# Kernel tuning notes

Hardware: AMD Instinct MI355X
Metric: run time of the kernel (lower is better)

## Reference

```python
import jax, jax.numpy as jnp
import numpy as np

N, D = 8192, 1024


def setup_inputs() -> dict:
    key = jax.random.key(0)
    k1, k2 = jax.random.split(key)
    x = jax.random.normal(k1, (N, D), dtype=jnp.float32)
    # scale weight like a trained linear layer (~1/sqrt(D)) so softmax isn't fully saturated
    W = jax.random.normal(k2, (D, D), dtype=jnp.float32) * (1.0 / np.sqrt(D))
    b = jnp.zeros((D,), dtype=jnp.float32)
    recency_weight = jnp.full((1,), -0.5, dtype=jnp.float32)  # nn.Parameter init in source
    return {"x": x, "W": W, "b": b, "recency_weight": recency_weight}


def reference(x, W, b, recency_weight):
    # linear + relu
    x_proj = jax.nn.relu(x @ W.T + b)          # [N, D]
    # tied self-matmul
    scores = x_proj @ x_proj.T                  # [N, N]
    n = x.shape[0]
    idx = jnp.arange(n)
    # causal mask: upper triangle strictly above diagonal (use_current_timestep=True)
    upper = idx[None, :] > idx[:, None]         # [N, N] bool
    scores = jnp.where(upper, -jnp.inf, scores)
    # recency bias: toeplitz |i - j|, zeroed on masked (upper) part, scaled by recency_weight
    dist = jnp.abs(idx[:, None] - idx[None, :]).astype(scores.dtype)
    recency = recency_weight[0] * jnp.where(upper, 0.0, dist)
    scores = scores + recency
    return jax.nn.softmax(scores, axis=1)       # [N, N] lower-triangular attention
```

## Files before the change

### kernel.cpp

```cpp
#include <hip/hip_runtime.h>
#include <math.h>

#define NR 8192
#define DIM 1024

typedef __attribute__((ext_vector_type(8))) short bf16x8;
typedef __attribute__((ext_vector_type(4))) float f32x4;

static __device__ __forceinline__ unsigned short f2bf(float f) {
  unsigned int u = __float_as_uint(f);
  u += 0x7fffu + ((u >> 16) & 1u);
  return (unsigned short)(u >> 16);
}

static __device__ __forceinline__ float bf2f(unsigned short u) {
  return __uint_as_float(((unsigned int)u) << 16);
}

static __device__ __forceinline__ void gload_lds16(const void* g, void* lds) {
  __builtin_amdgcn_global_load_lds(
      (const __attribute__((address_space(1))) unsigned int*)g,
      (__attribute__((address_space(3))) unsigned int*)lds, 16, 0, 0);
}

__global__ __launch_bounds__(256) void zerok(float* __restrict__ p, int n) {
  int i = blockIdx.x * 256 + threadIdx.x;
  if (i < n) p[i] = 0.0f;
}

__global__ __launch_bounds__(256) void cvt_bf16(const float* __restrict__ in,
                                                unsigned short* __restrict__ outp,
                                                int n4) {
  int i = blockIdx.x * 256 + threadIdx.x;
  if (i < n4) {
    float4 v = ((const float4*)in)[i];
    ushort4 o;
    o.x = f2bf(v.x); o.y = f2bf(v.y); o.z = f2bf(v.z); o.w = f2bf(v.w);
    ((ushort4*)outp)[i] = o;
  }
}

static __device__ __forceinline__ void gemm_core(const unsigned short* A,
                                                 const unsigned short* B,
                                                 int m0, int n0, int K,
                                                 short* As, short* Bs,
                                                 f32x4 acc[4][4]) {
  const int tid  = threadIdx.x;
  const int lane = tid & 63;
  const int wave = tid >> 6;
  const int wr = wave >> 1, wc = wave & 1;
  const int ch_r = lane >> 2;
  const int ch_c = (lane & 3) * 8;

  for (int kt = 0; kt < K; kt += 32) {
#pragma unroll
    for (int c = 0; c < 4; ++c) {
      int ch = wave * 4 + c;
      if (ch < 8) {
        const unsigned short* g = A + (size_t)(m0 + ch * 16 + ch_r) * DIM + kt + ch_c;
        gload_lds16(g, As + ch * 512);
      } else {
        const unsigned short* g = B + (size_t)(n0 + (ch - 8) * 16 + ch_r) * DIM + kt + ch_c;
        gload_lds16(g, Bs + (ch - 8) * 512);
      }
    }
    asm volatile("s_waitcnt vmcnt(0)" ::: "memory");
    __syncthreads();

    bf16x8 af[4], bfr[4];
#pragma unroll
    for (int m = 0; m < 4; ++m)
      af[m] = *(const bf16x8*)(As + (wr * 64 + m * 16 + (lane & 15)) * 32 + (lane >> 4) * 8);
#pragma unroll
    for (int n = 0; n < 4; ++n)
      bfr[n] = *(const bf16x8*)(Bs + (wc * 64 + n * 16 + (lane & 15)) * 32 + (lane >> 4) * 8);
#pragma unroll
    for (int m = 0; m < 4; ++m)
#pragma unroll
      for (int n = 0; n < 4; ++n)
        acc[m][n] = __builtin_amdgcn_mfma_f32_16x16x32_bf16(af[m], bfr[n], acc[m][n], 0, 0, 0);
    __syncthreads();
  }
}

__global__ __launch_bounds__(256) void gemm1_relu(const unsigned short* __restrict__ Xb,
                                                  const unsigned short* __restrict__ Wb,
                                                  const float* __restrict__ bias,
                                                  unsigned short* __restrict__ XP,
                                                  float* __restrict__ diag) {
  __shared__ short As[4096], Bs[4096];
  const int m0 = blockIdx.y * 128, n0 = blockIdx.x * 128;
  f32x4 acc[4][4] = {};
  gemm_core(Xb, Wb, m0, n0, DIM, As, Bs, acc);

  const int lane = threadIdx.x & 63, wave = threadIdx.x >> 6;
  const int wr = wave >> 1, wc = wave & 1, g = lane >> 4, li = lane & 15;
  float bv[4];
#pragma unroll
  for (int n = 0; n < 4; ++n) bv[n] = bias[n0 + wc * 64 + n * 16 + li];
#pragma unroll
  for (int m = 0; m < 4; ++m) {
#pragma unroll
    for (int r = 0; r < 4; ++r) {
      int row = m0 + wr * 64 + m * 16 + g * 4 + r;
      float ds = 0.0f;
#pragma unroll
      for (int n = 0; n < 4; ++n) {
        int col = n0 + wc * 64 + n * 16 + li;
        float v = fmaxf(acc[m][n][r] + bv[n], 0.0f);
        XP[(size_t)row * DIM + col] = f2bf(v);
        ds += v * v;
      }
#pragma unroll
      for (int off = 1; off < 16; off <<= 1) ds += __shfl_xor(ds, off);
      if (li == 0) atomicAdd(&diag[row], ds);
    }
  }
}

__global__ __launch_bounds__(256) void gemm2_scores(const unsigned short* __restrict__ XP,
                                                    const float* __restrict__ rwp,
                                                    unsigned short* __restrict__ Pb,
                                                    const float* __restrict__ diag,
                                                    float* __restrict__ Lrow) {
  int t = ((int)blockIdx.x & 7) * 260 + ((int)blockIdx.x >> 3);
  int by = (int)((sqrtf(8.0f * (float)t + 1.0f) - 1.0f) * 0.5f);
  while ((by + 1) * (by + 2) / 2 <= t) ++by;
  while (by * (by + 1) / 2 > t) --by;
  const int bx = t - by * (by + 1) / 2;

  __shared__ short As[4096], Bs[4096];
  const int m0 = by * 128, n0 = bx * 128;
  f32x4 acc[4][4] = {};
  gemm_core(XP, XP, m0, n0, DIM, As, Bs, acc);

  const float rw = rwp[0];
  const int lane = threadIdx.x & 63, wave = threadIdx.x >> 6;
  const int wr = wave >> 1, wc = wave & 1, g = lane >> 4, li = lane & 15;

#pragma unroll
  for (int m = 0; m < 4; ++m) {
#pragma unroll
    for (int r = 0; r < 4; ++r) {
      const int row = m0 + wr * 64 + m * 16 + g * 4 + r;
      const float dg = diag[row];
      float se = 0.0f;
#pragma unroll
      for (int n = 0; n < 4; ++n) {
        int col = n0 + wc * 64 + n * 16 + li;
        float v = acc[m][n][r];
        v = (col <= row) ? v + rw * (float)(row - col) : -INFINITY;
        float e = __expf(v - dg);
        se += e;
        if (col <= row) Pb[(size_t)row * NR + col] = f2bf(e);
      }
#pragma unroll
      for (int off = 1; off < 16; off <<= 1) se += __shfl_xor(se, off);
      if (li == 0) atomicAdd(&Lrow[row], se);
    }
  }
}

__global__ __launch_bounds__(256) void normk(const unsigned short* __restrict__ Pb,
                                             float* __restrict__ out,
                                             const float* __restrict__ Lrow) {
  const size_t idx = (size_t)blockIdx.x * 256 + threadIdx.x;
  const int row = (int)(idx >> 11);
  const int j0 = (int)(idx & 2047) * 4;
  float4* p = (float4*)out + idx;
  if (j0 > row) {
    float4 z; z.x = 0.f; z.y = 0.f; z.z = 0.f; z.w = 0.f;
    *p = z;
    return;
  }
  const float sc = __builtin_amdgcn_rcpf(Lrow[row]);
  ushort4 q = *(const ushort4*)(Pb + (size_t)row * NR + j0);
  float4 o;
  o.x = bf2f(q.x) * sc;
  o.y = bf2f(q.y) * sc;
  o.z = bf2f(q.z) * sc;
  o.w = bf2f(q.w) * sc;
  if (j0 + 3 > row) {
    if (j0 + 1 > row) o.y = 0.f;
    if (j0 + 2 > row) o.z = 0.f;
    o.w = 0.f;
  }
  *p = o;
}

extern "C" void kernel_launch(void* const* d_in, const int* in_sizes, int n_in,
                              void* d_out, int out_size, void* d_ws, size_t ws_size,
                              hipStream_t stream) {
  const float* x  = (const float*)d_in[0];
  const float* W  = (const float*)d_in[1];
  const float* b  = (const float*)d_in[2];
  const float* rw = (const float*)d_in[3];
  float* out = (float*)d_out;

  char* ws = (char*)d_ws;
  unsigned short* Xb = (unsigned short*)(ws);
  unsigned short* Wb = (unsigned short*)(ws + (size_t)(16 << 20));
  unsigned short* XP = (unsigned short*)(ws + (size_t)(18 << 20));
  float* diag = (float*)(ws + (size_t)(34 << 20));
  float* Lrow = (float*)(ws + (size_t)(34 << 20) + 32768);
  unsigned short* Pb = (unsigned short*)(ws + (size_t)(64 << 20));

  zerok<<<(2 * NR + 255) / 256, 256, 0, stream>>>(diag, 2 * NR);
  cvt_bf16<<<NR * DIM / 4 / 256, 256, 0, stream>>>(x, Xb, NR * DIM / 4);
  cvt_bf16<<<DIM * DIM / 4 / 256, 256, 0, stream>>>(W, Wb, DIM * DIM / 4);
  gemm1_relu<<<dim3(DIM / 128, NR / 128), 256, 0, stream>>>(Xb, Wb, b, XP, diag);
  gemm2_scores<<<2080, 256, 0, stream>>>(XP, rw, Pb, diag, Lrow);
  normk<<<(NR / 4) * (NR / 256), 256, 0, stream>>>(Pb, out, Lrow);
}
```

Measured before the change: 460.7 us.

## Add 4-stage async LDS pipeline with XOR swizzle to GEMM core

Replaces the single-buffered GEMM main loop with a 4-buffer ring that keeps three K-tiles of direct global-to-LDS loads in flight. Waits use partial vmcnt values and one barrier per iteration instead of a full drain plus two syncs. LDS chunks are XOR-swizzled on both the store and read sides to reduce bank conflicts. LDS use rises to 64KB per block, which may lower occupancy.

```diff
diff --git a/kernel.cpp b/kernel.cpp
--- a/kernel.cpp
+++ b/kernel.cpp
@@ -3,6 +3,7 @@
 
 #define NR 8192
 #define DIM 1024
+#define BK 32
 
 typedef __attribute__((ext_vector_type(8))) short bf16x8;
 typedef __attribute__((ext_vector_type(4))) float f32x4;
@@ -40,47 +41,62 @@
   }
 }
 
-static __device__ __forceinline__ void gemm_core(const unsigned short* A,
-                                                 const unsigned short* B,
-                                                 int m0, int n0, int K,
-                                                 short* As, short* Bs,
-                                                 f32x4 acc[4][4]) {
+static __device__ __forceinline__ void gemm_core_pipe(const unsigned short* A,
+                                                      const unsigned short* B,
+                                                      int m0, int n0,
+                                                      short* S,
+                                                      f32x4 acc[4][4]) {
   const int tid  = threadIdx.x;
   const int lane = tid & 63;
   const int wave = tid >> 6;
   const int wr = wave >> 1, wc = wave & 1;
-  const int ch_r = lane >> 2;
-  const int ch_c = (lane & 3) * 8;
-
-  for (int kt = 0; kt < K; kt += 32) {
-#pragma unroll
-    for (int c = 0; c < 4; ++c) {
-      int ch = wave * 4 + c;
-      if (ch < 8) {
-        const unsigned short* g = A + (size_t)(m0 + ch * 16 + ch_r) * DIM + kt + ch_c;
-        gload_lds16(g, As + ch * 512);
-      } else {
-        const unsigned short* g = B + (size_t)(n0 + (ch - 8) * 16 + ch_r) * DIM + kt + ch_c;
-        gload_lds16(g, Bs + (ch - 8) * 512);
-      }
-    }
-    asm volatile("s_waitcnt vmcnt(0)" ::: "memory");
-    __syncthreads();
-
+  const int li = lane & 15, g = lane >> 4;
+  const int r_loc = tid >> 2;
+  const int q     = (tid & 3) ^ ((r_loc >> 1) & 3);
+  const int kch = (g ^ ((li >> 1) & 3)) * 8;
+
+#define ISSUE_TILE(t_)                                                              \
+  do {                                                                              \
+    const int kt_ = (t_) * BK;                                                      \
+    short* buf_ = S + ((t_) & 3) * 8192;                                            \
+    gload_lds16(A + (size_t)(m0 +      r_loc) * DIM + kt_ + q * 8,                  \
+                buf_ + wave * 512);                                                 \
+    gload_lds16(A + (size_t)(m0 + 64 + r_loc) * DIM + kt_ + q * 8,                  \
+                buf_ + 2048 + wave * 512);                                          \
+    gload_lds16(B + (size_t)(n0 +      r_loc) * DIM + kt_ + q * 8,                  \
+                buf_ + 4096 + wave * 512);                                          \
+    gload_lds16(B + (size_t)(n0 + 64 + r_loc) * DIM + kt_ + q * 8,                  \
+                buf_ + 6144 + wave * 512);                                          \
+  } while (0)
+
+  ISSUE_TILE(0);
+  ISSUE_TILE(1);
+  ISSUE_TILE(2);
+
+  for (int t = 0; t < DIM / BK; ++t) {
+    if (t <= DIM / BK - 3)      asm volatile("s_waitcnt vmcnt(8)" ::: "memory");
+    else if (t == DIM / BK - 2) asm volatile("s_waitcnt vmcnt(4)" ::: "memory");
+    else                        asm volatile("s_waitcnt vmcnt(0)" ::: "memory");
+    __builtin_amdgcn_s_barrier();
+
+    const short* Ab = S + (t & 3) * 8192;
+    const short* Bb = Ab + 4096;
     bf16x8 af[4], bfr[4];
 #pragma unroll
     for (int m = 0; m < 4; ++m)
-      af[m] = *(const bf16x8*)(As + (wr * 64 + m * 16 + (lane & 15)) * 32 + (lane >> 4) * 8);
+      af[m] = *(const bf16x8*)(Ab + (wr * 64 + m * 16 + li) * 32 + kch);
 #pragma unroll
     for (int n = 0; n < 4; ++n)
-      bfr[n] = *(const bf16x8*)(Bs + (wc * 64 + n * 16 + (lane & 15)) * 32 + (lane >> 4) * 8);
+      bfr[n] = *(const bf16x8*)(Bb + (wc * 64 + n * 16 + li) * 32 + kch);
+    asm volatile("s_waitcnt lgkmcnt(0)" ::: "memory");
+    if (t + 3 < DIM / BK) ISSUE_TILE(t + 3);
 #pragma unroll
     for (int m = 0; m < 4; ++m)
 #pragma unroll
       for (int n = 0; n < 4; ++n)
         acc[m][n] = __builtin_amdgcn_mfma_f32_16x16x32_bf16(af[m], bfr[n], acc[m][n], 0, 0, 0);
-    __syncthreads();
-  }
+  }
+#undef ISSUE_TILE
 }
 
 __global__ __launch_bounds__(256) void gemm1_relu(const unsigned short* __restrict__ Xb,
@@ -88,10 +104,10 @@
                                                   const float* __restrict__ bias,
                                                   unsigned short* __restrict__ XP,
                                                   float* __restrict__ diag) {
-  __shared__ short As[4096], Bs[4096];
+  __shared__ short S[32768];
   const int m0 = blockIdx.y * 128, n0 = blockIdx.x * 128;
   f32x4 acc[4][4] = {};
-  gemm_core(Xb, Wb, m0, n0, DIM, As, Bs, acc);
+  gemm_core_pipe(Xb, Wb, m0, n0, S, acc);
 
   const int lane = threadIdx.x & 63, wave = threadIdx.x >> 6;
   const int wr = wave >> 1, wc = wave & 1, g = lane >> 4, li = lane & 15;
@@ -129,10 +145,10 @@
   while (by * (by + 1) / 2 > t) --by;
   const int bx = t - by * (by + 1) / 2;
 
-  __shared__ short As[4096], Bs[4096];
+  __shared__ short S[32768];
   const int m0 = by * 128, n0 = bx * 128;
   f32x4 acc[4][4] = {};
-  gemm_core(XP, XP, m0, n0, DIM, As, Bs, acc);
+  gemm_core_pipe(XP, XP, m0, n0, S, acc);
 
   const float rw = rwp[0];
   const int lane = threadIdx.x & 63, wave = threadIdx.x >> 6;
```

Result: no change. 461.1 us (+0.1%).
